# Optimization experiments

Measured on AMD Instinct MI355X. Metric: run time of the kernel, lower is better.

The kernel has to match this reference:

```python
import jax, jax.numpy as jnp
import numpy as np

D = 256          # object_dim == query_dim
HG = 1024        # g hidden / output width
HF0, HF1 = 1024, 512
OUT_F = 256
N = 32768        # number of objects


def _mlp_g(h, W0, b0, W1, b1, W2, b2):
    # g=True: ReLU after every layer, including output.
    h = jax.nn.relu(h @ W0 + b0)
    h = jax.nn.relu(h @ W1 + b1)
    return jax.nn.relu(h @ W2 + b2)


def _mlp_f(h, W0, b0, W1, b1, W2, b2):
    # f: ReLU on hidden layers, linear output.
    h = jax.nn.relu(h @ W0 + b0)
    h = jax.nn.relu(h @ W1 + b1)
    return h @ W2 + b2


def setup_inputs() -> dict:
    key = jax.random.key(0)
    ks = jax.random.split(key, 16)
    def lin(k, fan_in, fan_out):
        s = 1.0 / np.sqrt(fan_in)
        kw, kb = jax.random.split(k)
        W = jax.random.uniform(kw, (fan_in, fan_out), jnp.float32, -s, s)
        b = jax.random.uniform(kb, (fan_out,), jnp.float32, -s, s)
        return W, b
    x = jax.random.normal(ks[0], (N, D), jnp.float32)
    q = jax.random.normal(ks[1], (D,), jnp.float32)
    g_W0, g_b0 = lin(ks[2], 3 * D, HG)
    g_W1, g_b1 = lin(ks[3], HG, HG)
    g_W2, g_b2 = lin(ks[4], HG, HG)
    f_W0, f_b0 = lin(ks[5], HG, HF0)
    f_W1, f_b1 = lin(ks[6], HF0, HF1)
    f_W2, f_b2 = lin(ks[7], HF1, OUT_F)
    return dict(x=x, q=q,
                g_W0=g_W0, g_b0=g_b0, g_W1=g_W1, g_b1=g_b1, g_W2=g_W2, g_b2=g_b2,
                f_W0=f_W0, f_b0=f_b0, f_W1=f_W1, f_b1=f_b1, f_W2=f_W2, f_b2=f_b2)


def reference(x, q, g_W0, g_b0, g_W1, g_b1, g_W2, g_b2,
              f_W0, f_b0, f_W1, f_b1, f_W2, f_b2):
    n = x.shape[0]
    # mode 4: adjacent pairs (o_i, o_{i+1}), query concatenated to each pair.
    pair_concat = jnp.concatenate(
        [x[:-1], x[1:], jnp.broadcast_to(q, (n - 1, q.shape[0]))], axis=-1)  # (n-1, 3D)
    relations = _mlp_g(pair_concat, g_W0, g_b0, g_W1, g_b1, g_W2, g_b2)       # (n-1, HG)
    embedding = jnp.sum(relations, axis=0)                                     # (HG,)
    return _mlp_f(embedding, f_W0, f_b0, f_W1, f_b1, f_W2, f_b2)               # (OUT_F,)
```

## Files before the change

### kernel.cpp

```cpp
#include <hip/hip_runtime.h>

typedef __attribute__((ext_vector_type(8))) short short8;
typedef __attribute__((ext_vector_type(4))) float floatx4;
typedef __attribute__((ext_vector_type(4))) unsigned int uint32x4;

#define NROWS 32768L
#define NVALID 32767L
#define HGDIM 1024

__device__ __forceinline__ unsigned short f2bf_rne(float f) {
    union { float f; unsigned u; } v; v.f = f;
    unsigned r = v.u + 0x7fffu + ((v.u >> 16) & 1u);
    return (unsigned short)(r >> 16);
}

__device__ __forceinline__ void gload_lds16(const void* g, void* l) {
    __builtin_amdgcn_global_load_lds(
        (const __attribute__((address_space(1))) void*)g,
        (__attribute__((address_space(3))) void*)l,
        16, 0, 0);
}

#define NB_CVT 8193
#define NB_T0  512
#define NB_T1  1024
#define NB_T2  1024

__global__ void prep(const float* __restrict__ x, unsigned short* __restrict__ xb,
                     const float* __restrict__ gW0, unsigned short* __restrict__ w0t,
                     const float* __restrict__ gW1, unsigned short* __restrict__ w1t,
                     const float* __restrict__ gW2, unsigned short* __restrict__ w2t,
                     const float* __restrict__ q, const float* __restrict__ gb0,
                     float* __restrict__ c0) {
    __shared__ float smem[1056];
    int b = blockIdx.x, tid = threadIdx.x;
    if (b < NB_CVT) {
        long i = (long)b * 256 + tid;
        long ntot4 = (NROWS + 1) * 64;
        if (i < ntot4) {
            long i4 = i * 4, nx = NROWS * 256;
            float4 v = make_float4(0.f, 0.f, 0.f, 0.f);
            if (i4 < nx) v = *(const float4*)(x + i4);
            ushort4 o;
            o.x = f2bf_rne(v.x); o.y = f2bf_rne(v.y);
            o.z = f2bf_rne(v.z); o.w = f2bf_rne(v.w);
            *(ushort4*)(xb + i4) = o;
        }
        return;
    }
    b -= NB_CVT;
    const float* W; unsigned short* Wt; int K, N;
    if (b < NB_T0)                  { W = gW0; Wt = w0t; K = 512;  N = 1024; }
    else if (b < NB_T0 + NB_T1)     { b -= NB_T0; W = gW1; Wt = w1t; K = 1024; N = 1024; }
    else if (b < NB_T0 + NB_T1 + NB_T2) { b -= NB_T0 + NB_T1; W = gW2; Wt = w2t; K = 1024; N = 1024; }
    else {
        b -= NB_T0 + NB_T1 + NB_T2;
        int bx = b & 3, by = b >> 2;
        int j = bx * 256 + tid, k0 = by * 128;
        if (tid < 128) smem[tid] = q[k0 + tid];
        __syncthreads();
        float a = (by == 0) ? gb0[j] : 0.f;
        #pragma unroll 4
        for (int k = 0; k < 128; ++k)
            a += smem[k] * gW0[(size_t)(512 + k0 + k) * 1024 + j];
        atomicAdd(&c0[j], a);
        return;
    }
    int bx = b & 31, by = b >> 5;
    float (*tile)[33] = (float(*)[33])smem;
    int tx = tid & 31, ty = tid >> 5;
    int nb2 = bx * 32, kb = by * 32;
    #pragma unroll
    for (int i = 0; i < 32; i += 8)
        tile[ty + i][tx] = W[(size_t)(kb + ty + i) * N + (nb2 + tx)];
    __syncthreads();
    #pragma unroll
    for (int i = 0; i < 32; i += 8)
        Wt[(size_t)(nb2 + ty + i) * K + (kb + tx)] = f2bf_rne(tile[tx][ty + i]);
}

template<bool RELU_IN>
__global__ void fc_partial(const float* __restrict__ in, const float* __restrict__ W,
                           const float* __restrict__ bias, float* __restrict__ out,
                           int N) {
    __shared__ float s_in[128];
    int j = blockIdx.x * 256 + threadIdx.x;
    int k0 = blockIdx.y * 128;
    if (threadIdx.x < 128) {
        float v = in[k0 + threadIdx.x];
        if (RELU_IN) v = fmaxf(v, 0.f);
        s_in[threadIdx.x] = v;
    }
    __syncthreads();
    float acc = (blockIdx.y == 0) ? bias[j] : 0.f;
    #pragma unroll 4
    for (int k = 0; k < 128; ++k)
        acc += s_in[k] * W[(size_t)(k0 + k) * N + j];
    atomicAdd(&out[j], acc);
}


#define SBAR() __builtin_amdgcn_sched_barrier(0)

#define S_PRE() do { SBAR(); __builtin_amdgcn_s_barrier(); \
    asm volatile("s_waitcnt lgkmcnt(0)" ::: "memory"); SBAR(); \
    __builtin_amdgcn_s_setprio(1); } while (0)

#define S_POST() do { __builtin_amdgcn_s_setprio(0); SBAR(); \
    asm volatile("s_waitcnt vmcnt(2)" ::: "memory"); \
    __builtin_amdgcn_s_barrier(); } while (0)

#define STAGE(buf, region, T) do { \
    if ((region) >= 2) { \
        const unsigned short* _g = gA + (long)(((region) & 1) * 128) * lda + (long)(T) * 64; \
        char* _d = (char*)&lds[buf][0][((region) & 1) * 128][0] + t * 16; \
        gload_lds16(_g, _d); \
        gload_lds16(_g + 64L * lda, _d + 8192); \
    } else { \
        const unsigned short* _g = gB + (long)(((region) & 1) * 128) * ldb + (long)(T) * 64; \
        char* _d = (char*)&lds[buf][1][((region) & 1) * 128][0] + t * 16; \
        gload_lds16(_g, _d); \
        gload_lds16(_g + 64L * ldb, _d + 8192); \
    } } while (0)

#define LDA4(dst, buf, mbase, ks) do { _Pragma("unroll") for (int _q = 0; _q < 4; ++_q) \
    dst[_q] = *(const short8*)((const char*)&lds[buf][0][arowb + ((mbase) + _q) * 16][0] + ((ks) ? cb1 : cb0)); } while (0)

#define LDB4(dst, buf, ks) do { _Pragma("unroll") for (int _q = 0; _q < 4; ++_q) \
    dst[_q] = *(const short8*)((const char*)&lds[buf][1][browb + _q * 16][0] + ((ks) ? cb1 : cb0)); } while (0)

#define MFMA16(AF, BF, MO) do { _Pragma("unroll") for (int _mf = 0; _mf < 4; ++_mf) { \
    _Pragma("unroll") for (int _nf = 0; _nf < 4; ++_nf) \
        acc[(MO) + _mf][_nf] = __builtin_amdgcn_mfma_f32_16x16x32_bf16(AF[_mf], BF[_nf], acc[(MO) + _mf][_nf], 0, 0, 0); } } while (0)

template<int COLSUM>
__global__ __launch_bounds__(512, 2)
void gemmS(const unsigned short* __restrict__ A, int lda,
           const unsigned short* __restrict__ Bt, int ldb,
           const float* __restrict__ bias, int K,
           unsigned short* __restrict__ Hout,
           float* __restrict__ emb, long row0g, long nvalid,
           int mblocks) {
    __shared__ alignas(16) unsigned short lds[2][2][256][64];

    const int t = threadIdx.x;
    int nwg = gridDim.x, bid = blockIdx.x, swz;
    if ((nwg & 7) == 0) { int cpx = nwg >> 3; swz = (bid & 7) * cpx + (bid >> 3); }
    else swz = bid;
    const int mb = swz >> 2, nb = swz & 3;
    const long m0 = (long)mb * 256;
    const int n0 = nb * 256;

    const int srow = t >> 3;
    const int ssc = (t & 7) ^ (srow & 7);
    const unsigned short* gA = A + (m0 + srow) * (long)lda + ssc * 8;
    const unsigned short* gB = Bt + ((long)n0 + srow) * (long)ldb + ssc * 8;

    const int lane = t & 63;
    const int wv = t >> 6;
    const int wm = wv >> 2, wn = wv & 3;
    const int arowb = wm * 128 + (lane & 15);
    const int browb = wn * 64 + (lane & 15);
    const int c0x = (lane >> 4) ^ (lane & 7);
    const int cb0 = c0x * 16;
    const int cb1 = (c0x ^ 4) * 16;

    floatx4 acc[8][4] = {};

    const int NT = K >> 6;
    const int NI = NT >> 1;

    short8 bE0[4], bE1[4], bO0[4], bO1[4];
    short8 aE0[4], aE1[4], aE2[4], aE3[4], aO0[4], aO1[4], aO2[4], aO3[4];

    STAGE(0, 0, 0); STAGE(0, 1, 0); STAGE(0, 2, 0); STAGE(0, 3, 0);
    STAGE(1, 0, 1); STAGE(1, 1, 1);
    asm volatile("s_waitcnt vmcnt(4)" ::: "memory");
    SBAR();
    __builtin_amdgcn_s_barrier();
    SBAR();
    LDB4(bE0, 0, 0); LDA4(aE0, 0, 0, 0);

    for (int i = 0; i < NI; ++i) {
        const int O = 2 * i + 1;
        int N2 = 2 * i + 2; if (N2 >= NT) N2 = 0;
        int P2 = 2 * i + 3; if (P2 >= NT) P2 = 1;

        S_PRE();
        LDA4(aE1, 0, 4, 0);
        STAGE(1, 2, O);
        MFMA16(aE0, bE0, 0);
        S_POST();
        S_PRE();
        LDB4(bE1, 0, 1); LDA4(aE2, 0, 0, 1);
        STAGE(1, 3, O);
        MFMA16(aE1, bE0, 4);
        S_POST();
        S_PRE();
        LDA4(aE3, 0, 4, 1);
        STAGE(0, 0, N2);
        MFMA16(aE2, bE1, 0);
        S_POST();
        S_PRE();
        LDB4(bO0, 1, 0); LDA4(aO0, 1, 0, 0);
        STAGE(0, 1, N2);
        MFMA16(aE3, bE1, 4);
        S_POST();
        S_PRE();
        LDA4(aO1, 1, 4, 0);
        STAGE(0, 2, N2);
        MFMA16(aO0, bO0, 0);
        S_POST();
        S_PRE();
        LDB4(bO1, 1, 1); LDA4(aO2, 1, 0, 1);
        STAGE(0, 3, N2);
        MFMA16(aO1, bO0, 4);
        S_POST();
        S_PRE();
        LDA4(aO3, 1, 4, 1);
        STAGE(1, 0, P2);
        MFMA16(aO2, bO1, 0);
        S_POST();
        S_PRE();
        LDB4(bE0, 0, 0); LDA4(aE0, 0, 0, 0);
        STAGE(1, 1, P2);
        MFMA16(aO3, bO1, 4);
        S_POST();
    }
    asm volatile("s_waitcnt vmcnt(0) lgkmcnt(0)" ::: "memory");
    SBAR();
    __builtin_amdgcn_s_barrier();

    if (COLSUM == 0) {
        char* slb = (char*)&lds[0][0][0][0];
        #pragma unroll
        for (int nf = 0; nf < 4; ++nf) {
            int ncol = wn * 64 + nf * 16 + (lane & 15);
            float bv = bias[n0 + ncol];
            #pragma unroll
            for (int mf = 0; mf < 8; ++mf) {
                int rbase = wm * 128 + mf * 16 + ((lane >> 4) << 2);
                #pragma unroll
                for (int j = 0; j < 4; ++j) {
                    int row = rbase + j;
                    float v = fmaxf(acc[mf][nf][j] + bv, 0.f);
                    int byte = row * 512 + ((ncol * 2) ^ ((row & 7) << 4));
                    *(unsigned short*)(slb + byte) = f2bf_rne(v);
                }
            }
        }
        __syncthreads();
        {
            int rsub = t >> 5;
            int cb = (t & 31) * 16;
            #pragma unroll
            for (int i2 = 0; i2 < 16; ++i2) {
                int row = i2 * 16 + rsub;
                const char* src = slb + row * 512 + (cb ^ ((row & 7) << 4));
                uint32x4 v = *(const uint32x4*)src;
                char* dst = (char*)Hout + ((size_t)(m0 + row) * HGDIM + n0) * 2 + cb;
                *(uint32x4*)dst = v;
            }
        }
    } else {
        #pragma unroll
        for (int nf = 0; nf < 4; ++nf) {
            int ncol = n0 + wn * 64 + nf * 16 + (lane & 15);
            float bv = bias[ncol];
            float cs = 0.f;
            #pragma unroll
            for (int mf = 0; mf < 8; ++mf) {
                long rbase = row0g + m0 + wm * 128 + mf * 16 + ((lane >> 4) << 2);
                #pragma unroll
                for (int j = 0; j < 4; ++j) {
                    float v = fmaxf(acc[mf][nf][j] + bv, 0.f);
                    if (rbase + j < nvalid) cs += v;
                }
            }
            cs += __shfl_xor(cs, 16);
            cs += __shfl_xor(cs, 32);
            if ((lane >> 4) == 0) atomicAdd(&emb[ncol], cs);
        }
    }
}

extern "C" void kernel_launch(void* const* d_in, const int* in_sizes, int n_in,
                              void* d_out, int out_size, void* d_ws, size_t ws_size,
                              hipStream_t stream) {
    const float* x   = (const float*)d_in[0];
    const float* q   = (const float*)d_in[1];
    const float* gW0 = (const float*)d_in[2];
    const float* gb0 = (const float*)d_in[3];
    const float* gW1 = (const float*)d_in[4];
    const float* gb1 = (const float*)d_in[5];
    const float* gW2 = (const float*)d_in[6];
    const float* gb2 = (const float*)d_in[7];
    const float* fW0 = (const float*)d_in[8];
    const float* fb0 = (const float*)d_in[9];
    const float* fW1 = (const float*)d_in[10];
    const float* fb1 = (const float*)d_in[11];
    const float* fW2 = (const float*)d_in[12];
    const float* fb2 = (const float*)d_in[13];
    float* out = (float*)d_out;

    char* ws = (char*)d_ws;
    size_t off = 0;
    auto alloc = [&](size_t bytes) -> char* {
        char* p = ws + off;
        off += (bytes + 255) & ~(size_t)255;
        return p;
    };
    unsigned short* xb  = (unsigned short*)alloc((NROWS + 1) * 256 * 2);
    unsigned short* w0t = (unsigned short*)alloc((size_t)1024 * 512 * 2);
    unsigned short* w1t = (unsigned short*)alloc((size_t)1024 * 1024 * 2);
    unsigned short* w2t = (unsigned short*)alloc((size_t)1024 * 1024 * 2);
    float* c0  = (float*)alloc(4096);
    float* emb = (float*)alloc(4096);
    float* e1  = (float*)alloc(4096);
    float* e2  = (float*)alloc(4096);
    size_t fixed = off;
    size_t avail = (ws_size > fixed) ? ws_size - fixed : 0;
    long CR = (long)((avail / 2) / (HGDIM * 2));
    CR = (CR / 512) * 512;
    if (CR > NROWS) CR = NROWS;
    if (CR < 512) CR = 512;
    unsigned short* H0 = (unsigned short*)alloc((size_t)CR * HGDIM * 2);
    unsigned short* H1 = (unsigned short*)alloc((size_t)CR * HGDIM * 2);

    hipMemsetAsync(c0, 0, 4 * 4096, stream);
    hipMemsetAsync(out, 0, 256 * sizeof(float), stream);

    prep<<<dim3(NB_CVT + NB_T0 + NB_T1 + NB_T2 + 8), 256, 0, stream>>>(
        x, xb, gW0, w0t, gW1, w1t, gW2, w2t, q, gb0, c0);

    for (long r0 = 0; r0 < NROWS; r0 += CR) {
        long rows = NROWS - r0; if (rows > CR) rows = CR;
        int mblocks = (int)(rows / 256);
        dim3 g((unsigned)(mblocks * 4));
        gemmS<0><<<g, 512, 0, stream>>>(xb + r0 * 256, 256, w0t, 512, c0, 512,
                                        H0, nullptr, 0, 0, mblocks);
        gemmS<0><<<g, 512, 0, stream>>>(H0, 1024, w1t, 1024, gb1, 1024,
                                        H1, nullptr, 0, 0, mblocks);
        gemmS<1><<<g, 512, 0, stream>>>(H1, 1024, w2t, 1024, gb2, 1024,
                                        nullptr, emb, r0, NVALID, mblocks);
    }

    fc_partial<false><<<dim3(4, 8), 256, 0, stream>>>(emb, fW0, fb0, e1, 1024);
    fc_partial<true><<<dim3(2, 8), 256, 0, stream>>>(e1, fW1, fb1, e2, 512);
    fc_partial<true><<<dim3(1, 4), 256, 0, stream>>>(e2, fW2, fb2, out, 256);
}
```

Measured before the change: 231.0 us.

## Restructure GEMM main loop into four coarser phases with batched staging

The software-pipelined GEMM loop goes from eight barrier-separated phases per two K-tiles to four. Each phase now issues two MFMA groups and loads more LDS fragments, and global-to-LDS staging is regrouped with adjusted vmcnt waits. The aim is to halve the barrier and setprio overhead and to give each wave longer uninterrupted MFMA runs. The trade-off is coarser overlap between loads and compute, more live register fragments, and a riskier staging order that must not overwrite LDS still being read.

```diff
diff --git a/kernel.cpp b/kernel.cpp
--- a/kernel.cpp
+++ b/kernel.cpp
@@ -106,8 +106,8 @@
     asm volatile("s_waitcnt lgkmcnt(0)" ::: "memory"); SBAR(); \
     __builtin_amdgcn_s_setprio(1); } while (0)
 
-#define S_POST() do { __builtin_amdgcn_s_setprio(0); SBAR(); \
-    asm volatile("s_waitcnt vmcnt(2)" ::: "memory"); \
+#define S_POSTV(N) do { __builtin_amdgcn_s_setprio(0); SBAR(); \
+    asm volatile("s_waitcnt vmcnt(" #N ")" ::: "memory"); \
     __builtin_amdgcn_s_barrier(); } while (0)
 
 #define STAGE(buf, region, T) do { \
@@ -135,7 +135,7 @@
 
 template<int COLSUM>
 __global__ __launch_bounds__(512, 2)
-void gemmS(const unsigned short* __restrict__ A, int lda,
+void gemmT(const unsigned short* __restrict__ A, int lda,
            const unsigned short* __restrict__ Bt, int ldb,
            const float* __restrict__ bias, int K,
            unsigned short* __restrict__ Hout,
@@ -174,12 +174,12 @@
     short8 aE0[4], aE1[4], aE2[4], aE3[4], aO0[4], aO1[4], aO2[4], aO3[4];
 
     STAGE(0, 0, 0); STAGE(0, 1, 0); STAGE(0, 2, 0); STAGE(0, 3, 0);
-    STAGE(1, 0, 1); STAGE(1, 1, 1);
-    asm volatile("s_waitcnt vmcnt(4)" ::: "memory");
+    STAGE(1, 0, 1); STAGE(1, 2, 1); STAGE(1, 3, 1);
+    asm volatile("s_waitcnt vmcnt(6)" ::: "memory");
     SBAR();
     __builtin_amdgcn_s_barrier();
     SBAR();
-    LDB4(bE0, 0, 0); LDA4(aE0, 0, 0, 0);
+    LDB4(bE0, 0, 0); LDA4(aE0, 0, 0, 0); LDA4(aE1, 0, 4, 0);
 
     for (int i = 0; i < NI; ++i) {
         const int O = 2 * i + 1;
@@ -187,45 +187,25 @@
         int P2 = 2 * i + 3; if (P2 >= NT) P2 = 1;
 
         S_PRE();
-        LDA4(aE1, 0, 4, 0);
-        STAGE(1, 2, O);
-        MFMA16(aE0, bE0, 0);
-        S_POST();
+        LDB4(bE1, 0, 1); LDA4(aE2, 0, 0, 1); LDA4(aE3, 0, 4, 1);
+        STAGE(1, 1, O);
+        MFMA16(aE0, bE0, 0); MFMA16(aE1, bE0, 4);
+        S_POSTV(2);
         S_PRE();
-        LDB4(bE1, 0, 1); LDA4(aE2, 0, 0, 1);
-        STAGE(1, 3, O);
-        MFMA16(aE1, bE0, 4);
-        S_POST();
+        LDB4(bO0, 1, 0); LDA4(aO0, 1, 0, 0); LDA4(aO1, 1, 4, 0);
+        STAGE(0, 0, N2); STAGE(0, 2, N2); STAGE(0, 3, N2);
+        MFMA16(aE2, bE1, 0); MFMA16(aE3, bE1, 4);
+        S_POSTV(6);
         S_PRE();
-        LDA4(aE3, 0, 4, 1);
-        STAGE(0, 0, N2);
-        MFMA16(aE2, bE1, 0);
-        S_POST();
+        LDB4(bO1, 1, 1); LDA4(aO2, 1, 0, 1); LDA4(aO3, 1, 4, 1);
+        STAGE(0, 1, N2);
+        MFMA16(aO0, bO0, 0); MFMA16(aO1, bO0, 4);
+        S_POSTV(2);
         S_PRE();
-        LDB4(bO0, 1, 0); LDA4(aO0, 1, 0, 0);
-        STAGE(0, 1, N2);
-        MFMA16(aE3, bE1, 4);
-        S_POST();
-        S_PRE();
-        LDA4(aO1, 1, 4, 0);
-        STAGE(0, 2, N2);
-        MFMA16(aO0, bO0, 0);
-        S_POST();
-        S_PRE();
-        LDB4(bO1, 1, 1); LDA4(aO2, 1, 0, 1);
-        STAGE(0, 3, N2);
-        MFMA16(aO1, bO0, 4);
-        S_POST();
-        S_PRE();
-        LDA4(aO3, 1, 4, 1);
-        STAGE(1, 0, P2);
-        MFMA16(aO2, bO1, 0);
-        S_POST();
-        S_PRE();
-        LDB4(bE0, 0, 0); LDA4(aE0, 0, 0, 0);
-        STAGE(1, 1, P2);
-        MFMA16(aO3, bO1, 4);
-        S_POST();
+        LDB4(bE0, 0, 0); LDA4(aE0, 0, 0, 0); LDA4(aE1, 0, 4, 0);
+        STAGE(1, 0, P2); STAGE(1, 2, P2); STAGE(1, 3, P2);
+        MFMA16(aO2, bO1, 0); MFMA16(aO3, bO1, 4);
+        S_POSTV(6);
     }
     asm volatile("s_waitcnt vmcnt(0) lgkmcnt(0)" ::: "memory");
     SBAR();
@@ -337,11 +317,11 @@
         long rows = NROWS - r0; if (rows > CR) rows = CR;
         int mblocks = (int)(rows / 256);
         dim3 g((unsigned)(mblocks * 4));
-        gemmS<0><<<g, 512, 0, stream>>>(xb + r0 * 256, 256, w0t, 512, c0, 512,
+        gemmT<0><<<g, 512, 0, stream>>>(xb + r0 * 256, 256, w0t, 512, c0, 512,
                                         H0, nullptr, 0, 0, mblocks);
-        gemmS<0><<<g, 512, 0, stream>>>(H0, 1024, w1t, 1024, gb1, 1024,
+        gemmT<0><<<g, 512, 0, stream>>>(H0, 1024, w1t, 1024, gb1, 1024,
                                         H1, nullptr, 0, 0, mblocks);
-        gemmS<1><<<g, 512, 0, stream>>>(H1, 1024, w2t, 1024, gb2, 1024,
+        gemmT<1><<<g, 512, 0, stream>>>(H1, 1024, w2t, 1024, gb2, 1024,
                                         nullptr, emb, r0, NVALID, mblocks);
     }
 
```

Result: no change. 232.8 us (+0.8%).
